# Kernel optimization log

Measured on AMD Instinct MI355X. Metric: run time of the kernel, lower is better.

Reference implementation:

```python
import jax, jax.numpy as jnp
import numpy as np

N_NODES = 50000
N_EDGES = 800000
NUM_GRAPHS = 1024
IN_DIM = 25
DIM = 64
STEPS = 3


def setup_inputs() -> dict:
    key = jax.random.key(0)
    ks = jax.random.split(key, 16)
    s = 0.1
    return {
        "x": jax.random.normal(ks[0], (N_NODES, IN_DIM), dtype=jnp.float32),
        "edge_index": jax.random.randint(ks[1], (2, N_EDGES), 0, N_NODES),
        "batch": jnp.sort(jax.random.randint(ks[2], (N_NODES,), 0, NUM_GRAPHS)),
        "W0": jax.random.normal(ks[3], (IN_DIM, DIM), dtype=jnp.float32) * s,
        "b0": jnp.zeros((DIM,), jnp.float32),
        "Wc": jax.random.normal(ks[4], (DIM, DIM), dtype=jnp.float32) * s,
        "bc": jnp.zeros((DIM,), jnp.float32),
        "Wih": jax.random.normal(ks[5], (4 * DIM, 2 * DIM), dtype=jnp.float32) * s,
        "Whh": jax.random.normal(ks[6], (4 * DIM, DIM), dtype=jnp.float32) * s,
        "bih": jnp.zeros((4 * DIM,), jnp.float32),
        "bhh": jnp.zeros((4 * DIM,), jnp.float32),
        "W1": jax.random.normal(ks[7], (2 * DIM, DIM), dtype=jnp.float32) * s,
        "b1": jnp.zeros((DIM,), jnp.float32),
        "W2": jax.random.normal(ks[8], (DIM, 1), dtype=jnp.float32) * s,
        "b2": jnp.zeros((1,), jnp.float32),
    }


def _lstm_cell(xin, h, c, Wih, Whh, bih, bhh):
    gates = xin @ Wih.T + h @ Whh.T + bih + bhh  # [B, 4*DIM]
    i, f, g, o = jnp.split(gates, 4, axis=-1)
    i, f, o = jax.nn.sigmoid(i), jax.nn.sigmoid(f), jax.nn.sigmoid(o)
    g = jnp.tanh(g)
    c = f * c + i * g
    h = o * jnp.tanh(c)
    return h, c


def reference(x, edge_index, batch, W0, b0, Wc, bc, Wih, Whh, bih, bhh, W1, b1, W2, b2):
    n = x.shape[0]
    # lin0 + relu
    h = jax.nn.relu(x @ W0 + b0)
    # GCNConv: x @ W, add self loops, symmetric normalization, scatter-add
    hw = h @ Wc
    loops = jnp.arange(n, dtype=edge_index.dtype)
    row = jnp.concatenate([edge_index[0], loops])  # sources
    col = jnp.concatenate([edge_index[1], loops])  # targets
    deg = jax.ops.segment_sum(jnp.ones_like(row, dtype=hw.dtype), col, num_segments=n)
    dinv = jnp.where(deg > 0, jax.lax.rsqrt(deg), 0.0)
    norm = dinv[row] * dinv[col]
    msg = hw[row] * norm[:, None]  # [E+N, DIM] gather
    agg = jax.ops.segment_sum(msg, col, num_segments=n) + bc
    h = jax.nn.relu(agg)
    # Set2Set pooling with LSTM, 3 processing steps
    B = NUM_GRAPHS
    q_star = jnp.zeros((B, 2 * DIM), h.dtype)
    hs = jnp.zeros((B, DIM), h.dtype)
    cs = jnp.zeros((B, DIM), h.dtype)
    for _ in range(STEPS):
        hs, cs = _lstm_cell(q_star, hs, cs, Wih, Whh, bih, bhh)
        q = hs  # [B, DIM]
        e = jnp.sum(h * q[batch], axis=-1)  # [N]
        emax = jax.ops.segment_max(e, batch, num_segments=B)
        a = jnp.exp(e - emax[batch])
        asum = jax.ops.segment_sum(a, batch, num_segments=B)
        a = a / asum[batch]
        r = jax.ops.segment_sum(a[:, None] * h, batch, num_segments=B)  # [B, DIM]
        q_star = jnp.concatenate([q, r], axis=-1)
    out = jax.nn.relu(q_star @ W1 + b1)
    out = out @ W2 + b2
    return out.reshape(-1)
```

## Files before the change

### kernel.cpp

```cpp
#include <hip/hip_runtime.h>
#include <hip/hip_fp16.h>
#include <math.h>

#define N_NODES 50000
#define N_EDGES 800000
#define NGRAPH  1024
#define IN_DIM  25
#define DIM     64

#define NBK 98
#define CAP 12288
#define NPB 128
#define NFILL (NBK * 4)
#define NBIN 391

__device__ inline float wsum(float v) {
#pragma unroll
  for (int off = 32; off > 0; off >>= 1) v += __shfl_xor(v, off, 64);
  return v;
}
__device__ inline int wsumi(int v) {
#pragma unroll
  for (int off = 32; off > 0; off >>= 1) v += __shfl_xor(v, off, 64);
  return v;
}
__device__ inline float sigmoidf(float x) { return 1.f / (1.f + expf(-x)); }

__global__ __launch_bounds__(256) void k_bin(const int* __restrict__ ei,
    int* __restrict__ gcur, int* __restrict__ pairs,
    const float* __restrict__ Wih, const float* __restrict__ Whh,
    float* __restrict__ WT) {
  __shared__ int hist[NBK];
  __shared__ int sbase[NBK];
  __shared__ int lbase[NBK];
  __shared__ int sorted[2048];
  int t = threadIdx.x;
  if (blockIdx.x == NBIN) {
    for (int i = t; i < 3 * DIM * 4 * DIM; i += 256) {
      int k = i >> 8, tt = i & 255;
      WT[i] = (k < 2 * DIM) ? Wih[tt * 2 * DIM + k] : Whh[tt * DIM + (k - 2 * DIM)];
    }
    return;
  }
  int base = blockIdx.x * 2048;
  for (int i = t; i < NBK; i += 256) hist[i] = 0;
  __syncthreads();
  int pk[8], bkt[8], rank[8];
#pragma unroll
  for (int k = 0; k < 8; k++) {
    int e = base + k * 256 + t;
    if (e < N_EDGES) {
      int row = ei[e];
      int col = ei[N_EDGES + e];
      int b = col >> 9;
      bkt[k] = b;
      rank[k] = atomicAdd(&hist[b], 1);
      pk[k] = (b << 25) | ((col & 511) << 16) | row;
    } else {
      bkt[k] = -1;
    }
  }
  __syncthreads();
  if (t < 64) {
    int i0 = 2 * t, i1 = 2 * t + 1;
    int v0 = (i0 < NBK) ? hist[i0] : 0;
    int v1 = (i1 < NBK) ? hist[i1] : 0;
    int loc = v0 + v1, x = loc;
#pragma unroll
    for (int d = 1; d < 64; d <<= 1) {
      int y = __shfl_up(x, d, 64);
      if (t >= d) x += y;
    }
    int excl = x - loc;
    if (i0 < NBK) sbase[i0] = excl;
    if (i1 < NBK) sbase[i1] = excl + v0;
  }
  __syncthreads();
#pragma unroll
  for (int k = 0; k < 8; k++)
    if (bkt[k] >= 0) sorted[sbase[bkt[k]] + rank[k]] = pk[k];
  for (int i = t; i < NBK; i += 256)
    lbase[i] = hist[i] ? atomicAdd(&gcur[i], hist[i]) : 0;
  __syncthreads();
  int ntot = min(2048, N_EDGES - base);
  for (int i = t; i < ntot; i += 256) {
    int p = sorted[i];
    int b = ((unsigned)p) >> 25;
    int gpos = lbase[b] + (i - sbase[b]);
    if (gpos < CAP) pairs[(size_t)b * CAP + gpos] = p & 0x1FFFFFF;
  }
}

__global__ __launch_bounds__(256) void k_fillcsr(const int* __restrict__ pairs,
    const int* __restrict__ gcur, int* __restrict__ cnt,
    float* __restrict__ dinv, int* __restrict__ adj) {
  __shared__ int hist[NPB];
  __shared__ int sbase, sbef;
  int b = blockIdx.x;
  int cb = b >> 2, sub = b & 3;
  int t = threadIdx.x, lane = t & 63;
  int lo = sub * NPB;
  int nb0 = cb * 512 + lo;
  if (t < NPB) hist[t] = 0;
  if (t == 0) { sbef = 0; sbase = 0; }
  __syncthreads();
  int ne = min(gcur[cb], CAP);
  const int* pp = pairs + (size_t)cb * CAP;
  int mybef = 0;
  for (int i = t; i < ne; i += 256) {
    int c = pp[i] >> 16;
    unsigned cl = (unsigned)(c - lo);
    if (cl < NPB) atomicAdd(&hist[cl], 1);
    mybef += (c < lo);
  }
  mybef = wsumi(mybef);
  if (lane == 0 && mybef) atomicAdd(&sbef, mybef);
  __syncthreads();
  if (t < NPB) {
    int node = nb0 + t;
    if (node < N_NODES) dinv[node] = rsqrtf((float)(hist[t] + 1));
  }
  if (t < 64) {
    int v = 0;
    for (int i = t; i < cb; i += 64) v += gcur[i];
    v = wsumi(v);
    if (t == 0) sbase = v;
  }
  __syncthreads();
  int basev = sbase + sbef;
  if (t < 64) {
    int v0 = hist[2 * t], v1 = hist[2 * t + 1];
    int loc = v0 + v1;
    int x = loc;
#pragma unroll
    for (int d = 1; d < 64; d <<= 1) {
      int y = __shfl_up(x, d, 64);
      if (t >= d) x += y;
    }
    int excl = basev + x - loc;
    hist[2 * t] = excl;
    hist[2 * t + 1] = excl + v0;
  }
  __syncthreads();
  if (t < NPB) {
    int node = nb0 + t;
    if (node < N_NODES) cnt[node] = hist[t];
  }
  if (b == NFILL - 1 && t == 0) cnt[N_NODES] = N_EDGES;
  __syncthreads();
  for (int i = t; i < ne; i += 256) {
    int p = pp[i];
    unsigned cl = (unsigned)((p >> 16) - lo);
    if (cl < NPB) {
      int slot = atomicAdd(&hist[cl], 1);
      adj[slot] = p & 0xFFFF;
    }
  }
}

__global__ __launch_bounds__(256) void k_lin0(const float* __restrict__ x,
    const float* __restrict__ W0, const float* __restrict__ b0,
    const float* __restrict__ Wc, const float* __restrict__ dinv,
    __half* __restrict__ hw16) {
  __shared__ float sx[64][IN_DIM + 1];
  __shared__ float sW0[IN_DIM][DIM];
  __shared__ float sh[64][DIM + 4];
  __shared__ float sWc[DIM][DIM];
  int t = threadIdx.x;
  int row0 = blockIdx.x * 64;
  for (int i = t; i < 64 * IN_DIM; i += 256) {
    int r = i / IN_DIM, k = i - r * IN_DIM;
    int row = row0 + r;
    sx[r][k] = (row < N_NODES) ? x[row * IN_DIM + k] : 0.f;
  }
  for (int i = t; i < IN_DIM * DIM; i += 256) sW0[i >> 6][i & 63] = W0[i];
  for (int i = t; i < DIM * DIM; i += 256) sWc[i >> 6][i & 63] = Wc[i];
  __syncthreads();
  int tc = (t & 15) * 4;
  int tr = (t >> 4) * 4;
  float acc[4][4];
  {
    float4 bb = *(const float4*)&b0[tc];
#pragma unroll
    for (int i = 0; i < 4; i++) {
      acc[i][0] = bb.x; acc[i][1] = bb.y; acc[i][2] = bb.z; acc[i][3] = bb.w;
    }
  }
#pragma unroll
  for (int k = 0; k < IN_DIM; k++) {
    float4 w = *(const float4*)&sW0[k][tc];
#pragma unroll
    for (int i = 0; i < 4; i++) {
      float a = sx[tr + i][k];
      acc[i][0] += a * w.x; acc[i][1] += a * w.y;
      acc[i][2] += a * w.z; acc[i][3] += a * w.w;
    }
  }
#pragma unroll
  for (int i = 0; i < 4; i++) {
    sh[tr + i][tc + 0] = fmaxf(acc[i][0], 0.f);
    sh[tr + i][tc + 1] = fmaxf(acc[i][1], 0.f);
    sh[tr + i][tc + 2] = fmaxf(acc[i][2], 0.f);
    sh[tr + i][tc + 3] = fmaxf(acc[i][3], 0.f);
  }
  __syncthreads();
#pragma unroll
  for (int i = 0; i < 4; i++) acc[i][0] = acc[i][1] = acc[i][2] = acc[i][3] = 0.f;
#pragma unroll 8
  for (int k = 0; k < DIM; k++) {
    float4 w = *(const float4*)&sWc[k][tc];
#pragma unroll
    for (int i = 0; i < 4; i++) {
      float a = sh[tr + i][k];
      acc[i][0] += a * w.x; acc[i][1] += a * w.y;
      acc[i][2] += a * w.z; acc[i][3] += a * w.w;
    }
  }
  float2* hwf2 = (float2*)hw16;
#pragma unroll
  for (int i = 0; i < 4; i++) {
    int row = row0 + tr + i;
    if (row < N_NODES) {
      float dv = dinv[row];
      float2 st;
      ((__half2*)&st)[0] = __floats2half2_rn(acc[i][0] * dv, acc[i][1] * dv);
      ((__half2*)&st)[1] = __floats2half2_rn(acc[i][2] * dv, acc[i][3] * dv);
      hwf2[(size_t)row * 16 + (t & 15)] = st;
    }
  }
}

__global__ __launch_bounds__(256) void k_gather(const int* __restrict__ adj,
    const int* __restrict__ cnt, const __half* __restrict__ hw16,
    const float* __restrict__ dinv, const float4* __restrict__ bc4,
    __half* __restrict__ h16) {
  int t = threadIdx.x;
  int lane = t & 63, wave = t >> 6;
  int q = lane >> 4, ql = lane & 15;
  int node = blockIdx.x * 16 + wave * 4 + q;
  if (node >= N_NODES) return;
  const float2* hwf2 = (const float2*)hw16;
  int s = cnt[node], eend = cnt[node + 1];
  float di = dinv[node];
  float4 a0 = make_float4(0.f, 0.f, 0.f, 0.f), a1 = a0, a2 = a0, a3 = a0;
  {
    float2 raw = hwf2[(size_t)node * 16 + ql];
    float2 f0 = __half22float2(((const __half2*)&raw)[0]);
    float2 f1 = __half22float2(((const __half2*)&raw)[1]);
    a0.x = f0.x; a0.y = f0.y; a0.z = f1.x; a0.w = f1.y;
  }
  int qb = q << 4;
  for (int cb = s; cb < eend; cb += 16) {
    int cn = min(16, eend - cb);
    int idx = (ql < cn) ? adj[cb + ql] : 0;
    int j = 0;
    for (; j + 4 <= cn; j += 4) {
      int r0 = __shfl(idx, qb + j, 64), r1 = __shfl(idx, qb + j + 1, 64);
      int r2 = __shfl(idx, qb + j + 2, 64), r3 = __shfl(idx, qb + j + 3, 64);
      float2 w0 = hwf2[(size_t)r0 * 16 + ql];
      float2 w1 = hwf2[(size_t)r1 * 16 + ql];
      float2 w2 = hwf2[(size_t)r2 * 16 + ql];
      float2 w3 = hwf2[(size_t)r3 * 16 + ql];
      float2 f;
      f = __half22float2(((const __half2*)&w0)[0]); a0.x += f.x; a0.y += f.y;
      f = __half22float2(((const __half2*)&w0)[1]); a0.z += f.x; a0.w += f.y;
      f = __half22float2(((const __half2*)&w1)[0]); a1.x += f.x; a1.y += f.y;
      f = __half22float2(((const __half2*)&w1)[1]); a1.z += f.x; a1.w += f.y;
      f = __half22float2(((const __half2*)&w2)[0]); a2.x += f.x; a2.y += f.y;
      f = __half22float2(((const __half2*)&w2)[1]); a2.z += f.x; a2.w += f.y;
      f = __half22float2(((const __half2*)&w3)[0]); a3.x += f.x; a3.y += f.y;
      f = __half22float2(((const __half2*)&w3)[1]); a3.z += f.x; a3.w += f.y;
    }
    for (; j < cn; j++) {
      int r = __shfl(idx, qb + j, 64);
      float2 w = hwf2[(size_t)r * 16 + ql];
      float2 f;
      f = __half22float2(((const __half2*)&w)[0]); a0.x += f.x; a0.y += f.y;
      f = __half22float2(((const __half2*)&w)[1]); a0.z += f.x; a0.w += f.y;
    }
  }
  float4 bb = bc4[ql];
  float ox = fmaxf(((a0.x + a1.x) + (a2.x + a3.x)) * di + bb.x, 0.f);
  float oy = fmaxf(((a0.y + a1.y) + (a2.y + a3.y)) * di + bb.y, 0.f);
  float oz = fmaxf(((a0.z + a1.z) + (a2.z + a3.z)) * di + bb.z, 0.f);
  float ow = fmaxf(((a0.w + a1.w) + (a2.w + a3.w)) * di + bb.w, 0.f);
  float2 st;
  ((__half2*)&st)[0] = __floats2half2_rn(ox, oy);
  ((__half2*)&st)[1] = __floats2half2_rn(oz, ow);
  ((float2*)h16)[(size_t)node * 16 + ql] = st;
}

__global__ __launch_bounds__(256) void k_set2set(
    const __half* __restrict__ h16, const int* __restrict__ batch,
    const float* __restrict__ WT, const float* __restrict__ bih,
    const float* __restrict__ bhh, const float* __restrict__ W1,
    const float* __restrict__ b1, const float* __restrict__ W2,
    const float* __restrict__ b2, float* __restrict__ out) {
  int b = blockIdx.x, t = threadIdx.x;
  int wave = t >> 6, lane = t & 63;
  int q = lane >> 4, ql = lane & 15;
  int qid = (wave << 2) + q;
  __shared__ float qs[2 * DIM];
  __shared__ float hsl[DIM], csl[DIM];
  __shared__ float gates[4 * DIM];
  __shared__ float red[16 * DIM];
  __shared__ float lred[16], wmax[16];
  __shared__ int seg[2];
  const float2* h2 = (const float2*)h16;
  if (t < 2) {
    int g = b + t;
    int lo = 0, hi = N_NODES;
    if (g == NGRAPH) lo = N_NODES;
    else while (lo < hi) { int mid = (lo + hi) >> 1; if (batch[mid] < g) lo = mid + 1; else hi = mid; }
    seg[t] = lo;
  }
  if (t < 2 * DIM) qs[t] = 0.f;
  if (t < DIM) { hsl[t] = 0.f; csl[t] = 0.f; }
  __syncthreads();
  int s = seg[0], eend = seg[1];
  float bsum = bih[t] + bhh[t];
  for (int step = 0; step < 3; step++) {
    float g = bsum;
    if (step > 0) {
      const float* wp = WT + t;
      float g1 = 0.f;
#pragma unroll 8
      for (int k = 0; k < 2 * DIM; k += 2) {
        g += qs[k] * wp[k * 4 * DIM];
        g1 += qs[k + 1] * wp[(k + 1) * 4 * DIM];
      }
#pragma unroll 8
      for (int k = 0; k < DIM; k += 2) {
        g += hsl[k] * wp[(2 * DIM + k) * 4 * DIM];
        g1 += hsl[k + 1] * wp[(2 * DIM + k + 1) * 4 * DIM];
      }
      g += g1;
    }
    gates[t] = g;
    __syncthreads();
    if (t < DIM) {
      float ig = sigmoidf(gates[t]);
      float fg = sigmoidf(gates[DIM + t]);
      float gg = tanhf(gates[2 * DIM + t]);
      float og = sigmoidf(gates[3 * DIM + t]);
      float c = fg * csl[t] + ig * gg;
      csl[t] = c;
      float hh = og * tanhf(c);
      hsl[t] = hh;
      qs[t] = hh;
    }
    __syncthreads();
    float4 qf = *(const float4*)&hsl[4 * ql];
    float m_w = -INFINITY, l_w = 0.f;
    float4 racc = make_float4(0.f, 0.f, 0.f, 0.f);
    for (int j = s + qid; j < eend; j += 16) {
      float2 raw = h2[(size_t)j * 16 + ql];
      float2 f0 = __half22float2(((const __half2*)&raw)[0]);
      float2 f1 = __half22float2(((const __half2*)&raw)[1]);
      float p = f0.x * qf.x + f0.y * qf.y + f1.x * qf.z + f1.y * qf.w;
#pragma unroll
      for (int off = 1; off < 16; off <<= 1) p += __shfl_xor(p, off, 64);
      float m_new = fmaxf(m_w, p);
      float scale = __expf(m_w - m_new);
      float a = __expf(p - m_new);
      racc.x = racc.x * scale + a * f0.x;
      racc.y = racc.y * scale + a * f0.y;
      racc.z = racc.z * scale + a * f1.x;
      racc.w = racc.w * scale + a * f1.y;
      l_w = l_w * scale + a;
      m_w = m_new;
    }
    *(float4*)&red[qid * DIM + 4 * ql] = racc;
    if (ql == 0) { lred[qid] = l_w; wmax[qid] = m_w; }
    __syncthreads();
    if (t < DIM) {
      float m_b = -1e30f;
      for (int i = 0; i < 16; i++) m_b = fmaxf(m_b, wmax[i]);
      float r = 0.f, l = 0.f;
      for (int i = 0; i < 16; i++) {
        float e = __expf(wmax[i] - m_b);
        r += red[i * DIM + t] * e;
        l += lred[i] * e;
      }
      qs[DIM + t] = (l > 0.f) ? r / l : 0.f;
    }
    __syncthreads();
  }
  if (t < DIM) {
    float acc = b1[t];
#pragma unroll
    for (int k = 0; k < 2 * DIM; k++) acc += qs[k] * W1[k * DIM + t];
    acc = fmaxf(acc, 0.f);
    float v = wsum(acc * W2[t]);
    if (t == 0) out[b] = v + b2[0];
  }
}

extern "C" void kernel_launch(void* const* d_in, const int* in_sizes, int n_in,
                              void* d_out, int out_size, void* d_ws, size_t ws_size,
                              hipStream_t stream) {
  const float* x    = (const float*)d_in[0];
  const int*   ei   = (const int*)d_in[1];
  const int*   batch= (const int*)d_in[2];
  const float* W0   = (const float*)d_in[3];
  const float* b0   = (const float*)d_in[4];
  const float* Wc   = (const float*)d_in[5];
  const float* bc   = (const float*)d_in[6];
  const float* Wih  = (const float*)d_in[7];
  const float* Whh  = (const float*)d_in[8];
  const float* bih  = (const float*)d_in[9];
  const float* bhh  = (const float*)d_in[10];
  const float* W1   = (const float*)d_in[11];
  const float* b1   = (const float*)d_in[12];
  const float* W2   = (const float*)d_in[13];
  const float* b2   = (const float*)d_in[14];
  float* out = (float*)d_out;

  __half* hw16 = (__half*)d_ws;
  __half* h16  = hw16 + (size_t)N_NODES * DIM;
  float* dinv  = (float*)(h16 + (size_t)N_NODES * DIM);
  float* WT    = dinv + N_NODES;
  int* cnt     = (int*)(WT + 3 * DIM * 4 * DIM);
  int* adj     = cnt + N_NODES + 2;
  int* gcur    = adj + N_EDGES;
  int* pairs   = gcur + NBK + 2;

  hipMemsetAsync(gcur, 0, NBK * sizeof(int), stream);
  k_bin<<<NBIN + 1, 256, 0, stream>>>(ei, gcur, pairs, Wih, Whh, WT);
  k_fillcsr<<<NFILL, 256, 0, stream>>>(pairs, gcur, cnt, dinv, adj);
  k_lin0<<<(N_NODES + 63) / 64, 256, 0, stream>>>(x, W0, b0, Wc, dinv, hw16);
  k_gather<<<(N_NODES + 15) / 16, 256, 0, stream>>>(adj, cnt, hw16, dinv,
                                                    (const float4*)bc, h16);
  k_set2set<<<NGRAPH, 256, 0, stream>>>(h16, batch, WT, bih, bhh, W1, b1, W2, b2, out);
}
```

Before: 209.4 us.

## Vectorize CSR fill reads, prefetch adjacency in gather, cache graph rows in LDS

k_fillcsr now reads the binned pairs as int4 in both its histogram and scatter passes, with a scalar tail loop. k_gather loads the next 16-entry adjacency chunk before processing the current one, which hides index-load latency. k_set2set copies up to 128 fp16 node rows of each graph into shared memory once and reuses them across the three attention steps instead of re-reading them from global memory. The adj offset is padded so the vector loads stay aligned. The risk is higher LDS use in set2set (16KB more) lowering occupancy, plus a little extra register pressure.

```diff
diff --git a/kernel.cpp b/kernel.cpp
--- a/kernel.cpp
+++ b/kernel.cpp
@@ -13,6 +13,7 @@
 #define NPB 128
 #define NFILL (NBK * 4)
 #define NBIN 391
+#define CROWS 128
 
 __device__ inline float wsum(float v) {
 #pragma unroll
@@ -106,11 +107,21 @@
   __syncthreads();
   int ne = min(gcur[cb], CAP);
   const int* pp = pairs + (size_t)cb * CAP;
+  const int4* pp4 = (const int4*)pp;
+  int ne4 = ne >> 2;
   int mybef = 0;
-  for (int i = t; i < ne; i += 256) {
+  for (int i = t; i < ne4; i += 256) {
+    int4 p4 = pp4[i];
+    int c0 = p4.x >> 16, c1 = p4.y >> 16, c2 = p4.z >> 16, c3 = p4.w >> 16;
+    if ((unsigned)(c0 - lo) < NPB) atomicAdd(&hist[c0 - lo], 1);
+    if ((unsigned)(c1 - lo) < NPB) atomicAdd(&hist[c1 - lo], 1);
+    if ((unsigned)(c2 - lo) < NPB) atomicAdd(&hist[c2 - lo], 1);
+    if ((unsigned)(c3 - lo) < NPB) atomicAdd(&hist[c3 - lo], 1);
+    mybef += (c0 < lo) + (c1 < lo) + (c2 < lo) + (c3 < lo);
+  }
+  for (int i = (ne4 << 2) + t; i < ne; i += 256) {
     int c = pp[i] >> 16;
-    unsigned cl = (unsigned)(c - lo);
-    if (cl < NPB) atomicAdd(&hist[cl], 1);
+    if ((unsigned)(c - lo) < NPB) atomicAdd(&hist[c - lo], 1);
     mybef += (c < lo);
   }
   mybef = wsumi(mybef);
@@ -148,7 +159,19 @@
   }
   if (b == NFILL - 1 && t == 0) cnt[N_NODES] = N_EDGES;
   __syncthreads();
-  for (int i = t; i < ne; i += 256) {
+  for (int i = t; i < ne4; i += 256) {
+    int4 p4 = pp4[i];
+#pragma unroll
+    for (int u = 0; u < 4; u++) {
+      int p = (&p4.x)[u];
+      unsigned cl = (unsigned)((p >> 16) - lo);
+      if (cl < NPB) {
+        int slot = atomicAdd(&hist[cl], 1);
+        adj[slot] = p & 0xFFFF;
+      }
+    }
+  }
+  for (int i = (ne4 << 2) + t; i < ne; i += 256) {
     int p = pp[i];
     unsigned cl = (unsigned)((p >> 16) - lo);
     if (cl < NPB) {
@@ -250,9 +273,13 @@
     a0.x = f0.x; a0.y = f0.y; a0.z = f1.x; a0.w = f1.y;
   }
   int qb = q << 4;
+  int idx = 0;
+  if (s < eend && ql < eend - s) idx = adj[s + ql];
   for (int cb = s; cb < eend; cb += 16) {
     int cn = min(16, eend - cb);
-    int idx = (ql < cn) ? adj[cb + ql] : 0;
+    int nb = cb + 16;
+    int nidx = 0;
+    if (nb < eend && ql < eend - nb) nidx = adj[nb + ql];
     int j = 0;
     for (; j + 4 <= cn; j += 4) {
       int r0 = __shfl(idx, qb + j, 64), r1 = __shfl(idx, qb + j + 1, 64);
@@ -278,6 +305,7 @@
       f = __half22float2(((const __half2*)&w)[0]); a0.x += f.x; a0.y += f.y;
       f = __half22float2(((const __half2*)&w)[1]); a0.z += f.x; a0.w += f.y;
     }
+    idx = nidx;
   }
   float4 bb = bc4[ql];
   float ox = fmaxf(((a0.x + a1.x) + (a2.x + a3.x)) * di + bb.x, 0.f);
@@ -300,6 +328,7 @@
   int wave = t >> 6, lane = t & 63;
   int q = lane >> 4, ql = lane & 15;
   int qid = (wave << 2) + q;
+  __shared__ float2 hcf2[CROWS * 16];
   __shared__ float qs[2 * DIM];
   __shared__ float hsl[DIM], csl[DIM];
   __shared__ float gates[4 * DIM];
@@ -318,6 +347,10 @@
   if (t < DIM) { hsl[t] = 0.f; csl[t] = 0.f; }
   __syncthreads();
   int s = seg[0], eend = seg[1];
+  int nc = min(eend - s, CROWS);
+  for (int i = t; i < nc * 16; i += 256)
+    hcf2[i] = h2[(size_t)(s + (i >> 4)) * 16 + (i & 15)];
+  __syncthreads();
   float bsum = bih[t] + bhh[t];
   for (int step = 0; step < 3; step++) {
     float g = bsum;
@@ -354,7 +387,9 @@
     float m_w = -INFINITY, l_w = 0.f;
     float4 racc = make_float4(0.f, 0.f, 0.f, 0.f);
     for (int j = s + qid; j < eend; j += 16) {
-      float2 raw = h2[(size_t)j * 16 + ql];
+      int lj = j - s;
+      float2 raw = (lj < CROWS) ? hcf2[lj * 16 + ql]
+                                : h2[(size_t)j * 16 + ql];
       float2 f0 = __half22float2(((const __half2*)&raw)[0]);
       float2 f1 = __half22float2(((const __half2*)&raw)[1]);
       float p = f0.x * qf.x + f0.y * qf.y + f1.x * qf.z + f1.y * qf.w;
@@ -421,7 +456,7 @@
   float* dinv  = (float*)(h16 + (size_t)N_NODES * DIM);
   float* WT    = dinv + N_NODES;
   int* cnt     = (int*)(WT + 3 * DIM * 4 * DIM);
-  int* adj     = cnt + N_NODES + 2;
+  int* adj     = cnt + N_NODES + 4;
   int* gcur    = adj + N_EDGES;
   int* pairs   = gcur + NBK + 2;
 
```

Result: faster. 199.7 us (-4.6%).
